# Performance work log

Measured on AMD Instinct MI355X. Metric: run time of the kernel, lower is better.

Reference implementation:

```python
import jax, jax.numpy as jnp
import numpy as np

# Inverse Haar synthesis filters [LL, LH, HL, HH], each 2x2, shape [4,2,2]
_INV_FILTERS = jnp.array([
    [[0.5, 0.5], [0.5, 0.5]],    # LL
    [[-0.5, -0.5], [0.5, 0.5]],  # LH
    [[-0.5, 0.5], [-0.5, 0.5]],  # HL
    [[0.5, -0.5], [-0.5, 0.5]],  # HH
], dtype=jnp.float32)


def _iwt(ll, hf, filt):
    # ll: [B,C,H,W]; hf: [B,3C,H,W] -> recon [B,C,2H,2W]
    B, C, H, W = ll.shape
    # interleave: per channel c -> [ll_c, hf_{3c..3c+2}*2-1], shape [B,C,4,H,W]
    res = jnp.concatenate([ll[:, :, None], hf.reshape(B, C, 3, H, W) * 2.0 - 1.0], axis=2)
    # stride-2 2x2 transpose conv == scatter each pixel into a 2x2 block
    out = jnp.einsum('bckhw,kpq->bchpwq', res, filt)  # [B,C,H,2,W,2]
    return out.reshape(B, C, 2 * H, 2 * W)


def setup_inputs() -> dict:
    key = jax.random.key(0)
    k1, k2, k3, k4 = jax.random.split(key, 4)
    B, in_ch = 16, 64
    fused = jax.random.normal(k1, (B, in_ch, 128, 128), dtype=jnp.float32)
    hf1 = jax.random.uniform(k2, (B, 9, 256, 256), dtype=jnp.float32)
    hf2 = jax.random.uniform(k3, (B, 9, 128, 128), dtype=jnp.float32)
    conv_w = jax.random.normal(k4, (3, in_ch, 3, 3), dtype=jnp.float32) * 0.05
    conv_b = jnp.zeros((3,), dtype=jnp.float32)
    return {"fused": fused, "hf1": hf1, "hf2": hf2, "conv_w": conv_w, "conv_b": conv_b}


def reference(fused, hf1, hf2, conv_w, conv_b):
    # recov: Conv2d(in_ch, 3, 3, padding=1) + Tanh
    y = jax.lax.conv_general_dilated(
        fused, conv_w, window_strides=(1, 1), padding=((1, 1), (1, 1)),
        dimension_numbers=('NCHW', 'OIHW', 'NCHW'))
    ll_ref = jnp.tanh(y + conv_b[None, :, None, None])  # [B,3,128,128]
    # multi_iwt over reversed coeffs: curr starts at coarsest ll (= ll_ref)
    curr = _iwt(ll_ref, hf2, _INV_FILTERS)  # [B,3,256,256]
    curr = _iwt(curr, hf1, _INV_FILTERS)    # [B,3,512,512]
    return curr
```

## Files before the change

### kernel.cpp

```cpp
#include <hip/hip_runtime.h>
#include <cmath>


#define H1 128
#define W1 128
#define H2 256
#define W2 256
#define H3 512
#define W3 512
#define IN_CH 64
#define NB 16
#define PLANE (H1 * W1)
#define LLSZ (NB * 3 * PLANE)

template <int ICP>
__global__ __launch_bounds__(256) void conv_part_kernel(
    const float* __restrict__ fused,
    const float* __restrict__ cw,
    float* __restrict__ part)
{
    const int tx    = threadIdx.x;
    const int ty    = threadIdx.y;
    const int chunk = blockIdx.x;
    const int h     = blockIdx.y * 4 + ty;
    const int b     = blockIdx.z;
    const int w0    = tx * 2;

    float acc[3][2];
    #pragma unroll
    for (int oc = 0; oc < 3; ++oc) { acc[oc][0] = 0.f; acc[oc][1] = 0.f; }

    const float* fc = fused + ((size_t)b * IN_CH + chunk * ICP) * PLANE;

    #pragma unroll 2
    for (int ic = 0; ic < ICP; ++ic) {
        const float* fp = fc + (size_t)ic * PLANE;
        float v[3][4];
        #pragma unroll
        for (int r = 0; r < 3; ++r) {
            const int hh = h + r - 1;
            const bool hv = ((unsigned)hh) < (unsigned)H1;
            const float* row = fp + hh * W1;
            v[r][0] = (hv && (w0 > 0)) ? row[w0 - 1] : 0.f;
            if (hv) {
                float2 m = *(const float2*)(row + w0);
                v[r][1] = m.x; v[r][2] = m.y;
            } else { v[r][1] = 0.f; v[r][2] = 0.f; }
            v[r][3] = (hv && ((w0 + 2) < W1)) ? row[w0 + 2] : 0.f;
        }
        #pragma unroll
        for (int oc = 0; oc < 3; ++oc) {
            const float* wp = cw + (oc * IN_CH + chunk * ICP + ic) * 9;
            #pragma unroll
            for (int kh = 0; kh < 3; ++kh) {
                #pragma unroll
                for (int kw = 0; kw < 3; ++kw) {
                    const float wv = wp[kh * 3 + kw];
                    acc[oc][0] = fmaf(v[kh][kw],     wv, acc[oc][0]);
                    acc[oc][1] = fmaf(v[kh][kw + 1], wv, acc[oc][1]);
                }
            }
        }
    }

    const size_t base = (size_t)chunk * LLSZ + (((size_t)b * 3) * H1 + h) * W1 + w0;
    #pragma unroll
    for (int oc = 0; oc < 3; ++oc) {
        float2 o; o.x = acc[oc][0]; o.y = acc[oc][1];
        *(float2*)(part + base + (size_t)oc * PLANE) = o;
    }
}

template <int NCHUNK>
__global__ __launch_bounds__(256) void iwt2_kernel(
    const float* __restrict__ part,
    const float* __restrict__ cb,
    const float* __restrict__ hf2,
    const float* __restrict__ hf1,
    float* __restrict__ out)
{
    const int idx = blockIdx.x * 256 + threadIdx.x;
    const int w0 = (idx & 63) * 2;
    const int h  = (idx >> 6) & (H1 - 1);
    const int rest = idx >> 13;
    const int c = rest % 3;
    const int b = rest / 3;

    const size_t llbase = (((size_t)(b * 3 + c)) * H1 + h) * W1 + w0;
    float sx = 0.f, sy = 0.f;
    #pragma unroll
    for (int k = 0; k < NCHUNK; ++k) {
        float2 p = *(const float2*)(part + (size_t)k * LLSZ + llbase);
        sx += p.x; sy += p.y;
    }
    const float bias = cb[c];
    float llv[2];
    llv[0] = tanhf(sx + bias);
    llv[1] = tanhf(sy + bias);

    const float* h2p = hf2 + (((size_t)b * 9 + 3 * c) * H1 + h) * W1 + w0;
    float mid[2][2][2];
    {
        const float2 A  = *(const float2*)(h2p);
        const float2 Bv = *(const float2*)(h2p + PLANE);
        const float2 Cv = *(const float2*)(h2p + 2 * PLANE);
        const float a[2]  = { A.x * 2.f - 1.f,  A.y * 2.f - 1.f };
        const float bq[2] = { Bv.x * 2.f - 1.f, Bv.y * 2.f - 1.f };
        const float cq[2] = { Cv.x * 2.f - 1.f, Cv.y * 2.f - 1.f };
        #pragma unroll
        for (int x = 0; x < 2; ++x) {
            mid[x][0][0] = 0.5f * (llv[x] - a[x] - bq[x] + cq[x]);
            mid[x][0][1] = 0.5f * (llv[x] - a[x] + bq[x] - cq[x]);
            mid[x][1][0] = 0.5f * (llv[x] + a[x] - bq[x] - cq[x]);
            mid[x][1][1] = 0.5f * (llv[x] + a[x] + bq[x] + cq[x]);
        }
    }

    const float* h1b = hf1 + ((size_t)b * 9 + 3 * c) * (H2 * W2);
    float* ob = out + ((size_t)(b * 3 + c)) * (H3 * W3);

    #pragma unroll
    for (int p = 0; p < 2; ++p) {
        const int Hr = 2 * h + p;
        const float* rowp = h1b + (size_t)Hr * W2 + 2 * w0;
        float4 A  = *(const float4*)(rowp);
        float4 Bv = *(const float4*)(rowp + H2 * W2);
        float4 Cv = *(const float4*)(rowp + 2 * H2 * W2);
        const float a[2][2]  = { {A.x * 2.f - 1.f,  A.y * 2.f - 1.f},  {A.z * 2.f - 1.f,  A.w * 2.f - 1.f} };
        const float bb[2][2] = { {Bv.x * 2.f - 1.f, Bv.y * 2.f - 1.f}, {Bv.z * 2.f - 1.f, Bv.w * 2.f - 1.f} };
        const float cc[2][2] = { {Cv.x * 2.f - 1.f, Cv.y * 2.f - 1.f}, {Cv.z * 2.f - 1.f, Cv.w * 2.f - 1.f} };
        #pragma unroll
        for (int r = 0; r < 2; ++r) {
            const float sr = r ? 1.f : -1.f;
            float* orow = ob + (size_t)(4 * h + 2 * p + r) * W3 + 4 * w0;
            #pragma unroll
            for (int x = 0; x < 2; ++x) {
                float4 o;
                o.x = 0.5f * (mid[x][p][0] + sr * a[x][0] - bb[x][0] - sr * cc[x][0]);
                o.y = 0.5f * (mid[x][p][0] + sr * a[x][0] + bb[x][0] + sr * cc[x][0]);
                o.z = 0.5f * (mid[x][p][1] + sr * a[x][1] - bb[x][1] - sr * cc[x][1]);
                o.w = 0.5f * (mid[x][p][1] + sr * a[x][1] + bb[x][1] + sr * cc[x][1]);
                *(float4*)(orow + 4 * x) = o;
            }
        }
    }
}

extern "C" void kernel_launch(void* const* d_in, const int* in_sizes, int n_in,
                              void* d_out, int out_size, void* d_ws, size_t ws_size,
                              hipStream_t stream) {
    (void)in_sizes; (void)n_in; (void)out_size;
    const float* fused = (const float*)d_in[0];
    const float* hf1   = (const float*)d_in[1];
    const float* hf2   = (const float*)d_in[2];
    const float* cw    = (const float*)d_in[3];
    const float* cb    = (const float*)d_in[4];
    float* out  = (float*)d_out;
    float* part = (float*)d_ws;

    const size_t need4 = (size_t)4 * LLSZ * sizeof(float);
    dim3 cblk(64, 4, 1);
    const int iwtBlocks = (NB * 3 * H1 * (W1 / 2)) / 256;

    if (ws_size >= need4) {
        dim3 cgrd(4, H1 / 4, NB);
        conv_part_kernel<16><<<cgrd, cblk, 0, stream>>>(fused, cw, part);
        iwt2_kernel<4><<<iwtBlocks, 256, 0, stream>>>(part, cb, hf2, hf1, out);
    } else {
        dim3 cgrd(1, H1 / 4, NB);
        conv_part_kernel<64><<<cgrd, cblk, 0, stream>>>(fused, cw, part);
        iwt2_kernel<1><<<iwtBlocks, 256, 0, stream>>>(part, cb, hf2, hf1, out);
    }
}
```

Baseline: 196.3 us.

## Split IWT into reduce-tanh pass and fine-grained per-row IWT kernel; shuffle conv halos

The convolution kernel now loads only its own float2 per row and gets the left and right neighbour pixels through wavefront shuffles, with a two-stage software prefetch of the next input channel. The partial-sum reduction and tanh move into a separate kernel that writes a materialized LL plane. The IWT kernel is remapped so each thread produces one float4 of a single output row, giving far more threads and contiguous stores. This adds an extra launch and an LL round-trip through the workspace, and the coarse-level hf2 and LL values are now reloaded by several threads.

New measurement: 169.1 us. 13.9% less time.

```diff
diff --git a/kernel.cpp b/kernel.cpp
--- a/kernel.cpp
+++ b/kernel.cpp
@@ -32,21 +32,28 @@
 
     const float* fc = fused + ((size_t)b * IN_CH + chunk * ICP) * PLANE;
 
-    #pragma unroll 2
-    for (int ic = 0; ic < ICP; ++ic) {
+    auto ld = [&](float2 m[3], int ic) {
         const float* fp = fc + (size_t)ic * PLANE;
+        #pragma unroll
+        for (int r = 0; r < 3; ++r) {
+            const int hh = h + r - 1;
+            if (((unsigned)hh) < (unsigned)H1) {
+                m[r] = *(const float2*)(fp + hh * W1 + w0);
+            } else {
+                m[r].x = 0.f; m[r].y = 0.f;
+            }
+        }
+    };
+
+    auto comp = [&](const float2 m[3], int ic) {
         float v[3][4];
         #pragma unroll
         for (int r = 0; r < 3; ++r) {
-            const int hh = h + r - 1;
-            const bool hv = ((unsigned)hh) < (unsigned)H1;
-            const float* row = fp + hh * W1;
-            v[r][0] = (hv && (w0 > 0)) ? row[w0 - 1] : 0.f;
-            if (hv) {
-                float2 m = *(const float2*)(row + w0);
-                v[r][1] = m.x; v[r][2] = m.y;
-            } else { v[r][1] = 0.f; v[r][2] = 0.f; }
-            v[r][3] = (hv && ((w0 + 2) < W1)) ? row[w0 + 2] : 0.f;
+            float left  = __shfl_up(m[r].y, 1, 64);
+            float right = __shfl_down(m[r].x, 1, 64);
+            if (tx == 0)  left = 0.f;
+            if (tx == 63) right = 0.f;
+            v[r][0] = left; v[r][1] = m[r].x; v[r][2] = m[r].y; v[r][3] = right;
         }
         #pragma unroll
         for (int oc = 0; oc < 3; ++oc) {
@@ -61,6 +68,15 @@
                 }
             }
         }
+    };
+
+    float2 A[3], B[3];
+    ld(A, 0);
+    for (int ic = 0; ic < ICP; ic += 2) {
+        ld(B, ic + 1);
+        comp(A, ic);
+        if (ic + 2 < ICP) ld(A, ic + 2);
+        comp(B, ic + 1);
     }
 
     const size_t base = (size_t)chunk * LLSZ + (((size_t)b * 3) * H1 + h) * W1 + w0;
@@ -71,79 +87,79 @@
     }
 }
 
+__global__ __launch_bounds__(256) void reduce_tanh_kernel(
+    const float* __restrict__ part,
+    const float* __restrict__ cb,
+    float* __restrict__ ll)
+{
+    const int j = blockIdx.x * 256 + threadIdx.x;
+    const int c = (j >> 12) % 3;
+    float4 s = *(const float4*)(part + 4 * (size_t)j);
+    #pragma unroll
+    for (int k = 1; k < 4; ++k) {
+        float4 p = *(const float4*)(part + (size_t)k * LLSZ + 4 * (size_t)j);
+        s.x += p.x; s.y += p.y; s.z += p.z; s.w += p.w;
+    }
+    const float bias = cb[c];
+    float4 o;
+    o.x = tanhf(s.x + bias); o.y = tanhf(s.y + bias);
+    o.z = tanhf(s.z + bias); o.w = tanhf(s.w + bias);
+    *(float4*)(ll + 4 * (size_t)j) = o;
+}
+
 template <int NCHUNK>
-__global__ __launch_bounds__(256) void iwt2_kernel(
-    const float* __restrict__ part,
+__global__ __launch_bounds__(256) void iwt_fine_kernel(
+    const float* __restrict__ llp,
     const float* __restrict__ cb,
     const float* __restrict__ hf2,
     const float* __restrict__ hf1,
     float* __restrict__ out)
 {
     const int idx = blockIdx.x * 256 + threadIdx.x;
-    const int w0 = (idx & 63) * 2;
-    const int h  = (idx >> 6) & (H1 - 1);
-    const int rest = idx >> 13;
+    const int k    = idx & 127;
+    const int H    = (idx >> 7) & 511;
+    const int rest = idx >> 16;
     const int c = rest % 3;
     const int b = rest / 3;
+    const int h  = H >> 2;
+    const int p  = (H >> 1) & 1;
+    const int r  = H & 1;
+    const int Hr = H >> 1;
 
-    const size_t llbase = (((size_t)(b * 3 + c)) * H1 + h) * W1 + w0;
-    float sx = 0.f, sy = 0.f;
-    #pragma unroll
-    for (int k = 0; k < NCHUNK; ++k) {
-        float2 p = *(const float2*)(part + (size_t)k * LLSZ + llbase);
-        sx += p.x; sy += p.y;
-    }
-    const float bias = cb[c];
-    float llv[2];
-    llv[0] = tanhf(sx + bias);
-    llv[1] = tanhf(sy + bias);
-
-    const float* h2p = hf2 + (((size_t)b * 9 + 3 * c) * H1 + h) * W1 + w0;
-    float mid[2][2][2];
-    {
-        const float2 A  = *(const float2*)(h2p);
-        const float2 Bv = *(const float2*)(h2p + PLANE);
-        const float2 Cv = *(const float2*)(h2p + 2 * PLANE);
-        const float a[2]  = { A.x * 2.f - 1.f,  A.y * 2.f - 1.f };
-        const float bq[2] = { Bv.x * 2.f - 1.f, Bv.y * 2.f - 1.f };
-        const float cq[2] = { Cv.x * 2.f - 1.f, Cv.y * 2.f - 1.f };
+    const size_t llidx = (((size_t)(b * 3 + c)) * H1 + h) * W1 + k;
+    float llv;
+    if constexpr (NCHUNK == 0) {
+        llv = llp[llidx];
+    } else {
+        float s = 0.f;
         #pragma unroll
-        for (int x = 0; x < 2; ++x) {
-            mid[x][0][0] = 0.5f * (llv[x] - a[x] - bq[x] + cq[x]);
-            mid[x][0][1] = 0.5f * (llv[x] - a[x] + bq[x] - cq[x]);
-            mid[x][1][0] = 0.5f * (llv[x] + a[x] - bq[x] - cq[x]);
-            mid[x][1][1] = 0.5f * (llv[x] + a[x] + bq[x] + cq[x]);
-        }
+        for (int kk = 0; kk < NCHUNK; ++kk) s += llp[(size_t)kk * LLSZ + llidx];
+        llv = tanhf(s + cb[c]);
     }
 
-    const float* h1b = hf1 + ((size_t)b * 9 + 3 * c) * (H2 * W2);
-    float* ob = out + ((size_t)(b * 3 + c)) * (H3 * W3);
+    const float* h2p = hf2 + (((size_t)(b * 9 + 3 * c)) * H1 + h) * W1 + k;
+    const float a2 = h2p[0]         * 2.f - 1.f;
+    const float b2 = h2p[PLANE]     * 2.f - 1.f;
+    const float c2 = h2p[2 * PLANE] * 2.f - 1.f;
+    const float sp = p ? 1.f : -1.f;
+    const float m0 = 0.5f * (llv + sp * a2 - b2 - sp * c2);
+    const float m1 = 0.5f * (llv + sp * a2 + b2 + sp * c2);
 
-    #pragma unroll
-    for (int p = 0; p < 2; ++p) {
-        const int Hr = 2 * h + p;
-        const float* rowp = h1b + (size_t)Hr * W2 + 2 * w0;
-        float4 A  = *(const float4*)(rowp);
-        float4 Bv = *(const float4*)(rowp + H2 * W2);
-        float4 Cv = *(const float4*)(rowp + 2 * H2 * W2);
-        const float a[2][2]  = { {A.x * 2.f - 1.f,  A.y * 2.f - 1.f},  {A.z * 2.f - 1.f,  A.w * 2.f - 1.f} };
-        const float bb[2][2] = { {Bv.x * 2.f - 1.f, Bv.y * 2.f - 1.f}, {Bv.z * 2.f - 1.f, Bv.w * 2.f - 1.f} };
-        const float cc[2][2] = { {Cv.x * 2.f - 1.f, Cv.y * 2.f - 1.f}, {Cv.z * 2.f - 1.f, Cv.w * 2.f - 1.f} };
-        #pragma unroll
-        for (int r = 0; r < 2; ++r) {
-            const float sr = r ? 1.f : -1.f;
-            float* orow = ob + (size_t)(4 * h + 2 * p + r) * W3 + 4 * w0;
-            #pragma unroll
-            for (int x = 0; x < 2; ++x) {
-                float4 o;
-                o.x = 0.5f * (mid[x][p][0] + sr * a[x][0] - bb[x][0] - sr * cc[x][0]);
-                o.y = 0.5f * (mid[x][p][0] + sr * a[x][0] + bb[x][0] + sr * cc[x][0]);
-                o.z = 0.5f * (mid[x][p][1] + sr * a[x][1] - bb[x][1] - sr * cc[x][1]);
-                o.w = 0.5f * (mid[x][p][1] + sr * a[x][1] + bb[x][1] + sr * cc[x][1]);
-                *(float4*)(orow + 4 * x) = o;
-            }
-        }
-    }
+    const float* h1p = hf1 + ((size_t)(b * 9 + 3 * c)) * (H2 * W2) + (size_t)Hr * W2 + 2 * k;
+    const float2 A  = *(const float2*)(h1p);
+    const float2 Bv = *(const float2*)(h1p + H2 * W2);
+    const float2 Cv = *(const float2*)(h1p + 2 * H2 * W2);
+    const float a0 = A.x  * 2.f - 1.f, a1 = A.y  * 2.f - 1.f;
+    const float b0 = Bv.x * 2.f - 1.f, b1 = Bv.y * 2.f - 1.f;
+    const float c0 = Cv.x * 2.f - 1.f, c1 = Cv.y * 2.f - 1.f;
+    const float sr = r ? 1.f : -1.f;
+
+    float4 o;
+    o.x = 0.5f * (m0 + sr * a0 - b0 - sr * c0);
+    o.y = 0.5f * (m0 + sr * a0 + b0 + sr * c0);
+    o.z = 0.5f * (m1 + sr * a1 - b1 - sr * c1);
+    o.w = 0.5f * (m1 + sr * a1 + b1 + sr * c1);
+    *(float4*)(out + (((size_t)(b * 3 + c)) * H3 + H) * W3 + 4 * k) = o;
 }
 
 extern "C" void kernel_launch(void* const* d_in, const int* in_sizes, int n_in,
@@ -158,17 +174,24 @@
     float* out  = (float*)d_out;
     float* part = (float*)d_ws;
 
-    const size_t need4 = (size_t)4 * LLSZ * sizeof(float);
+    const size_t need_part4 = (size_t)4 * LLSZ * sizeof(float);
+    const size_t need_full  = (size_t)5 * LLSZ * sizeof(float);
     dim3 cblk(64, 4, 1);
-    const int iwtBlocks = (NB * 3 * H1 * (W1 / 2)) / 256;
+    const int iwtBlocks = (NB * 3 * H3 * W3 / 4) / 256;
 
-    if (ws_size >= need4) {
+    if (ws_size >= need_full) {
+        float* ll = part + (size_t)4 * LLSZ;
         dim3 cgrd(4, H1 / 4, NB);
         conv_part_kernel<16><<<cgrd, cblk, 0, stream>>>(fused, cw, part);
-        iwt2_kernel<4><<<iwtBlocks, 256, 0, stream>>>(part, cb, hf2, hf1, out);
+        reduce_tanh_kernel<<<LLSZ / 4 / 256, 256, 0, stream>>>(part, cb, ll);
+        iwt_fine_kernel<0><<<iwtBlocks, 256, 0, stream>>>(ll, cb, hf2, hf1, out);
+    } else if (ws_size >= need_part4) {
+        dim3 cgrd(4, H1 / 4, NB);
+        conv_part_kernel<16><<<cgrd, cblk, 0, stream>>>(fused, cw, part);
+        iwt_fine_kernel<4><<<iwtBlocks, 256, 0, stream>>>(part, cb, hf2, hf1, out);
     } else {
         dim3 cgrd(1, H1 / 4, NB);
         conv_part_kernel<64><<<cgrd, cblk, 0, stream>>>(fused, cw, part);
-        iwt2_kernel<1><<<iwtBlocks, 256, 0, stream>>>(part, cb, hf2, hf1, out);
+        iwt_fine_kernel<1><<<iwtBlocks, 256, 0, stream>>>(part, cb, hf2, hf1, out);
     }
 }
```
